# Kernel optimization log

Measured on AMD Instinct MI355X. Metric: run time of the kernel, lower is better.

The kernel has to match this reference:

```python
import jax, jax.numpy as jnp
import numpy as np

N_EMBD = 1024
N_HEAD = 16
B, T = 2, 2048
EPS_LN = 1e-5
EPS_RENORM = 1e-8


def _layernorm(x, w, b):
    mu = jnp.mean(x, axis=-1, keepdims=True)
    var = jnp.mean(jnp.square(x - mu), axis=-1, keepdims=True)
    return (x - mu) * jax.lax.rsqrt(var + EPS_LN) * w + b


def setup_inputs() -> dict:
    key = jax.random.key(0)
    ks = jax.random.split(key, 8)
    C = N_EMBD
    s = 0.02
    return {
        "x": jax.random.normal(ks[0], (B, T, C), jnp.float32),
        "ln1_w": jnp.ones((C,), jnp.float32),
        "ln1_b": jnp.zeros((C,), jnp.float32),
        "w_attn": jax.random.normal(ks[1], (C, 3 * C), jnp.float32) * s,
        "b_attn": jnp.zeros((3 * C,), jnp.float32),
        "w_attn_proj": jax.random.normal(ks[2], (C, C), jnp.float32) * s,
        "b_attn_proj": jnp.zeros((C,), jnp.float32),
        "threshold": jnp.full((N_HEAD,), 0.01, jnp.float32),
        "leak": jnp.full((N_HEAD,), 2.0, jnp.float32),
        "steepness": jnp.full((N_HEAD,), 2.0, jnp.float32),
        "ln2_w": jnp.ones((C,), jnp.float32),
        "ln2_b": jnp.zeros((C,), jnp.float32),
        "w_fc": jax.random.normal(ks[3], (C, 4 * C), jnp.float32) * s,
        "b_fc": jnp.zeros((4 * C,), jnp.float32),
        "w_mlp_proj": jax.random.normal(ks[4], (4 * C, C), jnp.float32) * s,
        "b_mlp_proj": jnp.zeros((C,), jnp.float32),
    }


def _ember_block(x, ln1_w, ln1_b, w_attn, b_attn, w_attn_proj, b_attn_proj,
                 threshold, leak, steepness, ln2_w, ln2_b,
                 w_fc, b_fc, w_mlp_proj, b_mlp_proj):
    Bx, Tx, C = x.shape
    H = N_HEAD
    D = C // H

    h = _layernorm(x, ln1_w, ln1_b)
    qkv = h @ w_attn + b_attn                      # [B,T,3C]
    q, k, v = jnp.split(qkv, 3, axis=-1)
    q = q.reshape(Bx, Tx, H, D).transpose(0, 2, 1, 3)  # [B,H,T,D]
    k = k.reshape(Bx, Tx, H, D).transpose(0, 2, 1, 3)
    v = v.reshape(Bx, Tx, H, D).transpose(0, 2, 1, 3)

    att = jnp.einsum('bhqd,bhkd->bhqk', q, k) * (1.0 / np.sqrt(D))
    causal = jnp.tril(jnp.ones((Tx, Tx), bool))
    att = jnp.where(causal[None, None], att, -jnp.inf)
    p = jax.nn.softmax(att, axis=-1)               # [B,H,T,T]

    # per-head LIF gating
    th = (jnp.abs(threshold) * 0.1)[None, :, None, None]
    lk = jax.nn.sigmoid(leak)[None, :, None, None]
    st = jax.nn.softplus(steepness)[None, :, None, None]
    fire = jax.nn.sigmoid(st * (p - th))
    w = fire + lk * (1.0 - fire)
    m = p * w
    m = m / (jnp.sum(m, axis=-1, keepdims=True) + EPS_RENORM)

    y = jnp.einsum('bhqk,bhkd->bhqd', m, v)
    y = y.transpose(0, 2, 1, 3).reshape(Bx, Tx, C)
    y = y @ w_attn_proj + b_attn_proj
    x = x + y

    h2 = _layernorm(x, ln2_w, ln2_b)
    h2 = jax.nn.gelu(h2 @ w_fc + b_fc, approximate=False)
    x = x + (h2 @ w_mlp_proj + b_mlp_proj)
    return x


def reference(x, ln1_w, ln1_b, w_attn, b_attn, w_attn_proj, b_attn_proj,
              threshold, leak, steepness, ln2_w, ln2_b,
              w_fc, b_fc, w_mlp_proj, b_mlp_proj):
    return _ember_block(x, ln1_w, ln1_b, w_attn, b_attn, w_attn_proj, b_attn_proj,
                        threshold, leak, steepness, ln2_w, ln2_b,
                        w_fc, b_fc, w_mlp_proj, b_mlp_proj)
```

## Files before the change

### kernel.cpp

```cpp
#include <hip/hip_runtime.h>
#include <hip/hip_bf16.h>
#include <math.h>

typedef __bf16 bf16_t;
typedef __bf16 bf16x8 __attribute__((ext_vector_type(8)));
typedef __bf16 bf16x4 __attribute__((ext_vector_type(4)));
typedef float  f32x4  __attribute__((ext_vector_type(4)));
typedef unsigned int u32;

static constexpr int C_    = 1024;
static constexpr int NH    = 16;
static constexpr int DH    = 64;
static constexpr int BB    = 2;
static constexpr int TT    = 2048;
static constexpr int MROWS = BB * TT;
static constexpr float LOG2E = 1.4426950408889634f;

__device__ __forceinline__ void gload_lds16(const bf16_t* src, bf16_t* dst) {
  __builtin_amdgcn_global_load_lds(
      (const __attribute__((address_space(1))) u32*)(src),
      (__attribute__((address_space(3))) u32*)(dst),
      16, 0, 0);
}

__device__ __forceinline__ u32 cvt_pk_bf16(float a, float b) {
  u32 r;
  asm("v_cvt_pk_bf16_f32 %0, %1, %2" : "=v"(r) : "v"(a), "v"(b));
  return r;
}

__device__ __forceinline__ float fexp2(float x) {
#if __has_builtin(__builtin_amdgcn_exp2f)
  return __builtin_amdgcn_exp2f(x);
#else
  return exp2f(x);
#endif
}
__device__ __forceinline__ float frcp(float x) {
#if __has_builtin(__builtin_amdgcn_rcpf)
  return __builtin_amdgcn_rcpf(x);
#else
  return 1.0f / x;
#endif
}

__device__ __forceinline__ int sc_to_t(int s, int c) {
  if (s < 32)  return s;
  if (s < 64)  return 32 + (s - 32) * 2 + c;
  if (s < 96)  return 96 + (s - 64) * 3 + c;
  return 192 + (s - 96) * 4 + c;
}

__device__ __forceinline__ void item40_to_uc(int t, int& u, int& c) {
  if (t < 4)       { u = t;                c = 0; }
  else if (t < 12) { int v = t - 4;  u = 4  + (v >> 1); c = v & 1; }
  else if (t < 24) { int v = t - 12; u = 8  + v / 3;    c = v - 3 * (v / 3); }
  else             { int v = t - 24; u = 12 + (v >> 2); c = v & 3; }
}

__global__ __launch_bounds__(256) void ln_bf16(
    const float* __restrict__ x, const float* __restrict__ w,
    const float* __restrict__ b, bf16_t* __restrict__ out)
{
  const int row = blockIdx.x;
  const int tid = threadIdx.x;
  const float4 v = reinterpret_cast<const float4*>(x + (size_t)row * C_)[tid];
  float s  = v.x + v.y + v.z + v.w;
  float s2 = v.x*v.x + v.y*v.y + v.z*v.z + v.w*v.w;
#pragma unroll
  for (int m = 1; m < 64; m <<= 1) { s += __shfl_xor(s, m); s2 += __shfl_xor(s2, m); }
  __shared__ float red[8];
  const int wv = tid >> 6;
  if ((tid & 63) == 0) { red[wv] = s; red[4 + wv] = s2; }
  __syncthreads();
  s  = red[0] + red[1] + red[2] + red[3];
  s2 = red[4] + red[5] + red[6] + red[7];
  const float mu   = s * (1.0f / C_);
  const float rstd = rsqrtf(s2 * (1.0f / C_) - mu * mu + 1e-5f);
  const float4 wv4 = reinterpret_cast<const float4*>(w)[tid];
  const float4 bv4 = reinterpret_cast<const float4*>(b)[tid];
  bf16x4 o;
  o[0] = (bf16_t)((v.x - mu) * rstd * wv4.x + bv4.x);
  o[1] = (bf16_t)((v.y - mu) * rstd * wv4.y + bv4.y);
  o[2] = (bf16_t)((v.z - mu) * rstd * wv4.z + bv4.z);
  o[3] = (bf16_t)((v.w - mu) * rstd * wv4.w + bv4.w);
  *reinterpret_cast<bf16x4*>(out + (size_t)row * C_ + tid * 4) = o;
}

__global__ __launch_bounds__(256) void ln2_fuse(
    const float* __restrict__ p0, const bf16_t* __restrict__ p1,
    const float* __restrict__ xin, const float* __restrict__ pbias,
    const float* __restrict__ w, const float* __restrict__ b,
    float* __restrict__ x2out, bf16_t* __restrict__ out)
{
  const int row = blockIdx.x;
  const int tid = threadIdx.x;
  const size_t base = (size_t)row * C_ + tid * 4;
  const float4 v0 = *reinterpret_cast<const float4*>(p0 + base);
  const bf16x4 v1 = *reinterpret_cast<const bf16x4*>(p1 + base);
  const float4 xr = *reinterpret_cast<const float4*>(xin + base);
  const float4 pb = *reinterpret_cast<const float4*>(pbias + tid * 4);
  float4 v;
  v.x = v0.x + (float)v1[0] + pb.x + xr.x;
  v.y = v0.y + (float)v1[1] + pb.y + xr.y;
  v.z = v0.z + (float)v1[2] + pb.z + xr.z;
  v.w = v0.w + (float)v1[3] + pb.w + xr.w;
  *reinterpret_cast<float4*>(x2out + base) = v;

  float s  = v.x + v.y + v.z + v.w;
  float s2 = v.x*v.x + v.y*v.y + v.z*v.z + v.w*v.w;
#pragma unroll
  for (int m = 1; m < 64; m <<= 1) { s += __shfl_xor(s, m); s2 += __shfl_xor(s2, m); }
  __shared__ float red[8];
  const int wv = tid >> 6;
  if ((tid & 63) == 0) { red[wv] = s; red[4 + wv] = s2; }
  __syncthreads();
  s  = red[0] + red[1] + red[2] + red[3];
  s2 = red[4] + red[5] + red[6] + red[7];
  const float mu   = s * (1.0f / C_);
  const float rstd = rsqrtf(s2 * (1.0f / C_) - mu * mu + 1e-5f);
  const float4 wv4 = reinterpret_cast<const float4*>(w)[tid];
  const float4 bv4 = reinterpret_cast<const float4*>(b)[tid];
  bf16x4 o;
  o[0] = (bf16_t)((v.x - mu) * rstd * wv4.x + bv4.x);
  o[1] = (bf16_t)((v.y - mu) * rstd * wv4.y + bv4.y);
  o[2] = (bf16_t)((v.z - mu) * rstd * wv4.z + bv4.z);
  o[3] = (bf16_t)((v.w - mu) * rstd * wv4.w + bv4.w);
  *reinterpret_cast<bf16x4*>(out + base) = o;
}

__global__ __launch_bounds__(256) void combine3(
    float* __restrict__ out, const bf16_t* __restrict__ p1,
    const bf16_t* __restrict__ p2, const bf16_t* __restrict__ p3,
    const float* __restrict__ bias, const float* __restrict__ resid)
{
  const size_t idx = ((size_t)blockIdx.x * 256 + threadIdx.x) * 4;
  float4 o = *reinterpret_cast<const float4*>(out + idx);
  const bf16x4 a = *reinterpret_cast<const bf16x4*>(p1 + idx);
  const bf16x4 b = *reinterpret_cast<const bf16x4*>(p2 + idx);
  const bf16x4 c = *reinterpret_cast<const bf16x4*>(p3 + idx);
  const float4 r = *reinterpret_cast<const float4*>(resid + idx);
  const int col = (int)(idx & (C_ - 1));
  const float4 bv = *reinterpret_cast<const float4*>(bias + col);
  o.x += (float)a[0] + (float)b[0] + (float)c[0] + bv.x + r.x;
  o.y += (float)a[1] + (float)b[1] + (float)c[1] + bv.y + r.y;
  o.z += (float)a[2] + (float)b[2] + (float)c[2] + bv.z + r.z;
  o.w += (float)a[3] + (float)b[3] + (float)c[3] + bv.w + r.w;
  *reinterpret_cast<float4*>(out + idx) = o;
}

__global__ __launch_bounds__(256) void transpose_w(
    const float* __restrict__ in, bf16_t* __restrict__ out, int K, int N)
{
  __shared__ float tile[32][33];
  const int tx = threadIdx.x & 31, ty = threadIdx.x >> 5;
  const int n0 = blockIdx.x * 32, k0 = blockIdx.y * 32;
#pragma unroll
  for (int i = 0; i < 4; ++i)
    tile[ty + i * 8][tx] = in[(size_t)(k0 + ty + i * 8) * N + n0 + tx];
  __syncthreads();
#pragma unroll
  for (int i = 0; i < 4; ++i)
    out[(size_t)(n0 + ty + i * 8) * K + k0 + tx] = (bf16_t)tile[tx][ty + i * 8];
}

template<int EPI>
__global__ __launch_bounds__(512, 1) void gemmP(
    const bf16_t* __restrict__ A, const bf16_t* __restrict__ Bt,
    const float* __restrict__ bias, float* __restrict__ fout,
    bf16_t* __restrict__ bout0, bf16_t* __restrict__ bout1,
    bf16_t* __restrict__ bout2, int N, int Kc, int Kfull, int nbn)
{
  __shared__ bf16_t As[3][256 * 64];
  __shared__ bf16_t Bs[3][128 * 64];
  const int tid  = threadIdx.x;
  const int wave = tid >> 6, lane = tid & 63;
  const int r = lane & 15, g = lane >> 4;
  const int wm = wave >> 2, wn = wave & 3;

  const int cpx = gridDim.x >> 3;
  const int swz = (blockIdx.x & 7) * cpx + (blockIdx.x >> 3);
  const int bm = swz / nbn, bn = swz - bm * nbn;
  const int z  = blockIdx.z;
  const int k0 = z * Kc;

  const bf16_t* Abase = A  + (size_t)bm * 256 * Kfull + k0;
  const bf16_t* Bbase = Bt + (size_t)bn * 128 * Kfull + k0;

  f32x4 acc[8][2] = {};

  auto STG_A = [&](int buf, int kt, int pass) {
    const int idx = pass * 512 + tid;
    const int rr = idx >> 3, cc = idx & 7, gs = cc ^ (rr & 7);
    gload_lds16(Abase + (size_t)rr * Kfull + kt + gs * 8, &As[buf][idx * 8]);
  };
  auto STG_B = [&](int buf, int kt, int pass) {
    const int idx = pass * 512 + tid;
    const int rr = idx >> 3, cc = idx & 7, gs = cc ^ (rr & 7);
    gload_lds16(Bbase + (size_t)rr * Kfull + kt + gs * 8, &Bs[buf][idx * 8]);
  };
  auto STAGE6 = [&](int buf, int kt) {
    STG_A(buf, kt, 0); STG_A(buf, kt, 1);
    STG_A(buf, kt, 2); STG_A(buf, kt, 3);
    STG_B(buf, kt, 0); STG_B(buf, kt, 1);
  };

  const int NT = Kc >> 6;
  STAGE6(0, 0);
  STAGE6(1, 64);

  for (int t = 0; t < NT; ++t) {
    const int buf = t % 3;
    if (t + 1 < NT) asm volatile("s_waitcnt vmcnt(6)" ::: "memory");
    else            asm volatile("s_waitcnt vmcnt(0)" ::: "memory");
    __builtin_amdgcn_s_barrier();
    asm volatile("" ::: "memory");

    const bool pre = (t + 2 < NT);
    const int kn   = (t + 2) << 6;
    const int bnx  = (t + 2) % 3;

    bf16x8 bfr[2][2];
#pragma unroll
    for (int s2 = 0; s2 < 2; ++s2)
#pragma unroll
      for (int ni = 0; ni < 2; ++ni) {
        const int rr = wn * 32 + ni * 16 + r;
        bfr[s2][ni] = *reinterpret_cast<const bf16x8*>(
            &Bs[buf][rr * 64 + (((s2 << 2) | g) ^ (rr & 7)) * 8]);
      }
#pragma unroll
    for (int mh = 0; mh < 2; ++mh) {
      bf16x8 af[2][4];
#pragma unroll
      for (int s2 = 0; s2 < 2; ++s2)
#pragma unroll
        for (int mi = 0; mi < 4; ++mi) {
          const int rr = wm * 128 + (mh * 4 + mi) * 16 + r;
          af[s2][mi] = *reinterpret_cast<const bf16x8*>(
              &As[buf][rr * 64 + (((s2 << 2) | g) ^ (rr & 7)) * 8]);
        }
      if (pre) {
        if (mh == 0) { STG_A(bnx, kn, 0); STG_A(bnx, kn, 1); STG_A(bnx, kn, 2); }
        else         { STG_A(bnx, kn, 3); STG_B(bnx, kn, 0); STG_B(bnx, kn, 1); }
      }
      __builtin_amdgcn_s_setprio(1);
#pragma unroll
      for (int s2 = 0; s2 < 2; ++s2)
#pragma unroll
        for (int mi = 0; mi < 4; ++mi)
#pragma unroll
          for (int ni = 0; ni < 2; ++ni)
            acc[mh * 4 + mi][ni] = __builtin_amdgcn_mfma_f32_16x16x32_bf16(
                af[s2][mi], bfr[s2][ni], acc[mh * 4 + mi][ni], 0, 0, 0);
      __builtin_amdgcn_s_setprio(0);
    }
  }

#pragma unroll
  for (int mi = 0; mi < 8; ++mi) {
#pragma unroll
    for (int ni = 0; ni < 2; ++ni) {
      const int grow0 = bm * 256 + wm * 128 + mi * 16 + g * 4;
      const int gcol  = bn * 128 + wn * 32 + ni * 16 + r;
      const float bv = bias[gcol];
#pragma unroll
      for (int i = 0; i < 4; ++i) {
        const int grow = grow0 + i;
        const float v = acc[mi][ni][i] + bv;
        if constexpr (EPI == 0) {
          const int which = gcol >> 10;
          const int c0 = gcol & 1023;
          const int hh = c0 >> 6, dd = c0 & 63;
          const int bb = grow >> 11, tt = grow & 2047;
          if (which == 2)
            bout2[((size_t)(bb * NH + hh) * DH + dd) * TT + tt] = (bf16_t)v;
          else {
            bf16_t* dst = (which == 0) ? bout0 : bout1;
            dst[((size_t)(bb * NH + hh) * TT + tt) * DH + dd] = (bf16_t)v;
          }
        } else {
          const float gl = 0.5f * v * (1.0f + erff(v * 0.70710678118654752f));
          bout0[(size_t)grow * N + gcol] = (bf16_t)gl;
        }
      }
    }
  }
}

__global__ __launch_bounds__(256) void gemm_sk(
    const bf16_t* __restrict__ A, const bf16_t* __restrict__ Bt,
    float* __restrict__ fout, bf16_t* __restrict__ bout0,
    bf16_t* __restrict__ bout1, bf16_t* __restrict__ bout2,
    int M, int N, int Kc, int Kfull)
{
  constexpr int BM = 128, BN = 128, BK = 64;
  __shared__ bf16_t As[BM * BK];
  __shared__ bf16_t Bs[BN * BK];
  const int tid  = threadIdx.x;
  const int wave = tid >> 6, lane = tid & 63;
  const int r = lane & 15, g = lane >> 4;
  const int wm = wave >> 1, wn = wave & 1;
  const int bm = blockIdx.x, bn = blockIdx.y;
  const int z  = blockIdx.z;
  const int kstart = z * Kc;

  const bf16_t* Abase = A  + (size_t)bm * BM * Kfull;
  const bf16_t* Bbase = Bt + (size_t)bn * BN * Kfull;

  f32x4 acc[4][4] = {};

  for (int kt = kstart; kt < kstart + Kc; kt += BK) {
#pragma unroll
    for (int it = 0; it < 4; ++it) {
      const int c0 = it * 256 + wave * 64;
      const int idx = c0 + lane;
      const int rr = idx >> 3, cc = idx & 7;
      const int gs = cc ^ (rr & 7);
      gload_lds16(Abase + (size_t)rr * Kfull + kt + gs * 8, As + c0 * 8);
    }
#pragma unroll
    for (int it = 0; it < 4; ++it) {
      const int c0 = it * 256 + wave * 64;
      const int idx = c0 + lane;
      const int rr = idx >> 3, cc = idx & 7;
      const int gs = cc ^ (rr & 7);
      gload_lds16(Bbase + (size_t)rr * Kfull + kt + gs * 8, Bs + c0 * 8);
    }
    asm volatile("s_waitcnt vmcnt(0)" ::: "memory");
    __syncthreads();
#pragma unroll
    for (int s = 0; s < 2; ++s) {
      bf16x8 af[4], bfr[4];
#pragma unroll
      for (int mi = 0; mi < 4; ++mi) {
        const int rr = wm * 64 + mi * 16 + r;
        const int ch = (s * 4 + g) ^ (rr & 7);
        af[mi] = *reinterpret_cast<const bf16x8*>(&As[rr * BK + ch * 8]);
      }
#pragma unroll
      for (int ni = 0; ni < 4; ++ni) {
        const int rr = wn * 64 + ni * 16 + r;
        const int ch = (s * 4 + g) ^ (rr & 7);
        bfr[ni] = *reinterpret_cast<const bf16x8*>(&Bs[rr * BK + ch * 8]);
      }
#pragma unroll
      for (int mi = 0; mi < 4; ++mi)
#pragma unroll
        for (int ni = 0; ni < 4; ++ni)
          acc[mi][ni] = __builtin_amdgcn_mfma_f32_16x16x32_bf16(
              af[mi], bfr[ni], acc[mi][ni], 0, 0, 0);
    }
    __syncthreads();
  }

#pragma unroll
  for (int mi = 0; mi < 4; ++mi) {
#pragma unroll
    for (int ni = 0; ni < 4; ++ni) {
      const int grow0 = bm * BM + wm * 64 + mi * 16 + g * 4;
      const int gcol  = bn * BN + wn * 64 + ni * 16 + r;
#pragma unroll
      for (int i = 0; i < 4; ++i) {
        const int grow = grow0 + i;
        const float v = acc[mi][ni][i];
        const size_t o = (size_t)grow * N + gcol;
        if (z == 0) fout[o] = v;
        else {
          bf16_t* pb = (z == 1) ? bout0 : (z == 2) ? bout1 : bout2;
          pb[o] = (bf16_t)v;
        }
      }
    }
  }
}


__global__ __launch_bounds__(512, 4) void attn_p1(
    const bf16_t* __restrict__ Q, const bf16_t* __restrict__ Km,
    float2* __restrict__ mzP)
{
  __shared__ bf16_t Ks[2][64 * 64];
  const int tid = threadIdx.x;
  const int w = tid >> 6, lane = tid & 63;
  const int r = lane & 15, g = lane >> 4;
  const int bid = blockIdx.x;
  const int bh  = (bid & 7) * 4 + ((bid >> 3) & 3);
  int gu, c; item40_to_uc(bid >> 5, gu, c);
  const int cmax = gu >> 2;
  const bool diag = (c == cmax);
  const int nt = diag ? ((gu & 3) * 2 + 2) : 8;
  const int s = gu * 8 + w;
  const int qrow = gu * 128 + w * 16 + r;

  const bf16_t* Qh = Q  + (size_t)bh * TT * DH;
  const bf16_t* Kh = Km + (size_t)bh * TT * DH;
  const float SCL = 0.125f * LOG2E;

  bf16x8 qf[2];
#pragma unroll
  for (int s2 = 0; s2 < 2; ++s2) {
    bf16x8 t = *reinterpret_cast<const bf16x8*>(Qh + (size_t)qrow * DH + s2 * 32 + g * 8);
#pragma unroll
    for (int i = 0; i < 8; ++i) t[i] = (bf16_t)((float)t[i] * SCL);
    qf[s2] = t;
  }

  auto STAGEK = [&](int b, int t8) {
    const int rr = tid >> 3, cc = tid & 7, gs = cc ^ (rr & 7);
    gload_lds16(Kh + (size_t)(c * 512 + t8 * 64 + rr) * DH + gs * 8, &Ks[b][tid * 8]);
  };

  float runM = -1e30f, runZ = 0.f;
  STAGEK(0, 0);
  for (int t8 = 0; t8 < nt; ++t8) {
    const int b = t8 & 1;
    asm volatile("s_waitcnt vmcnt(0)" ::: "memory");
    __syncthreads();
    if (t8 + 1 < nt) STAGEK(b ^ 1, t8 + 1);
    f32x4 sfT[4] = {};
#pragma unroll
    for (int s2 = 0; s2 < 2; ++s2) {
      bf16x8 kf[4];
#pragma unroll
      for (int ni = 0; ni < 4; ++ni)
        kf[ni] = *reinterpret_cast<const bf16x8*>(
            &Ks[b][(ni * 16 + r) * 64 + (((s2 << 2) | g) ^ (r & 7)) * 8]);
#pragma unroll
      for (int ni = 0; ni < 4; ++ni)
        sfT[ni] = __builtin_amdgcn_mfma_f32_16x16x32_bf16(kf[ni], qf[s2], sfT[ni], 0, 0, 0);
    }
    const int kbase = c * 512 + t8 * 64;
    float xv[16];
#pragma unroll
    for (int ni = 0; ni < 4; ++ni)
#pragma unroll
      for (int j = 0; j < 4; ++j) {
        float x = sfT[ni][j];
        if (diag) {
          const int kcol = kbase + ni * 16 + g * 4 + j;
          if (kcol > qrow) x = -1e30f;
        }
        xv[ni * 4 + j] = x;
      }
    float nm = runM;
#pragma unroll
    for (int e = 0; e < 16; ++e) nm = fmaxf(nm, xv[e]);
    float z = runZ * fexp2(runM - nm);
#pragma unroll
    for (int e = 0; e < 16; ++e) z += fexp2(xv[e] - nm);
    runM = nm; runZ = z;
  }
#pragma unroll
  for (int msk = 16; msk < 64; msk <<= 1) {
    const float om = __shfl_xor(runM, msk), oz = __shfl_xor(runZ, msk);
    const float nm = fmaxf(runM, om);
    runZ = runZ * fexp2(runM - nm) + oz * fexp2(om - nm);
    runM = nm;
  }
  if (lane < 16)
    mzP[((size_t)(bh * 128 + s) * 4 + c) * 16 + r] = make_float2(runM, runZ);
}

__global__ __launch_bounds__(512, 2) void attn_p3(
    const bf16_t* __restrict__ Q, const bf16_t* __restrict__ Km,
    const bf16_t* __restrict__ Vt, const float2* __restrict__ mzP,
    bf16_t* __restrict__ Y, uint2* __restrict__ yaccA,
    uint2* __restrict__ yaccB, float* __restrict__ denP,
    const float* __restrict__ thrp, const float* __restrict__ leakp,
    const float* __restrict__ steepp)
{
  __shared__ bf16_t Ks[2][64 * 64];
  __shared__ bf16_t Vs[2][64 * 64];
  __shared__ __align__(16) u32 Ms[8][512];

  const int tid = threadIdx.x;
  const int w = tid >> 6, lane = tid & 63;
  const int r = lane & 15, g = lane >> 4;
  const int bid = blockIdx.x;
  const int bh  = (bid & 7) * 4 + ((bid >> 3) & 3);
  int gu, c; item40_to_uc(bid >> 5, gu, c);
  const int cmax = gu >> 2;
  const bool diag = (c == cmax);
  const int nt = diag ? ((gu & 3) * 2 + 2) : 8;
  const int nch = cmax + 1;
  const int s = gu * 8 + w;
  const int row0w = gu * 128 + w * 16;
  const int qrow = row0w + r;
  const int hh = bh & (NH - 1), bb = bh >> 4;

  const bf16_t* Qh  = Q  + (size_t)bh * TT * DH;
  const bf16_t* Kh  = Km + (size_t)bh * TT * DH;
  const bf16_t* Vth = Vt + (size_t)bh * TT * DH;

  const float lk  = 1.0f / (1.0f + expf(-leakp[hh]));
  const float ilk = 1.0f - lk;
  const float st  = log1pf(expf(steepp[hh]));
  const float Lst = LOG2E * st;
  const float A0  = Lst * (fabsf(thrp[hh]) * 0.1f);

  float M = -1e30f, Z = 0.f;
  for (int c2 = 0; c2 < nch; ++c2) {
    const float2 mz = mzP[((size_t)(bh * 128 + s) * 4 + c2) * 16 + r];
    const float nm = fmaxf(M, mz.x);
    Z = Z * fexp2(M - nm) + mz.y * fexp2(mz.x - nm);
    M = nm;
  }
  const float rcpZ = frcp(Z);

  const float SCL = 0.125f * LOG2E;
  bf16x8 qf[2];
#pragma unroll
  for (int s2 = 0; s2 < 2; ++s2) {
    bf16x8 t = *reinterpret_cast<const bf16x8*>(Qh + (size_t)qrow * DH + s2 * 32 + g * 8);
#pragma unroll
    for (int i = 0; i < 8; ++i) t[i] = (bf16_t)((float)t[i] * SCL);
    qf[s2] = t;
  }
  bf16x8 ones;
#pragma unroll
  for (int i = 0; i < 8; ++i) ones[i] = (bf16_t)1.0f;

  uint2* MsU2 = reinterpret_cast<uint2*>(&Ms[w][0]);
  uint4* MsU4 = reinterpret_cast<uint4*>(&Ms[w][0]);

  auto STAGE = [&](int b, int t8) {
    const int kbase = c * 512 + t8 * 64;
    const int rr = tid >> 3, cc = tid & 7, gs = cc ^ (rr & 7);
    gload_lds16(Kh + (size_t)(kbase + rr) * DH + gs * 8, &Ks[b][tid * 8]);
    gload_lds16(Vth + (size_t)rr * TT + kbase + gs * 8, &Vs[b][tid * 8]);
  };

  f32x4 yacc[4] = {};
  f32x4 dacc = {};

  STAGE(0, 0);
  for (int t8 = 0; t8 < nt; ++t8) {
    const int b = t8 & 1;
    asm volatile("s_waitcnt vmcnt(0)" ::: "memory");
    __syncthreads();
    if (t8 + 1 < nt) STAGE(b ^ 1, t8 + 1);
    const int kbase = c * 512 + t8 * 64;
    f32x4 sfT[4] = {};
#pragma unroll
    for (int s2 = 0; s2 < 2; ++s2) {
      bf16x8 kf[4];
#pragma unroll
      for (int ni = 0; ni < 4; ++ni)
        kf[ni] = *reinterpret_cast<const bf16x8*>(
            &Ks[b][(ni * 16 + r) * 64 + (((s2 << 2) | g) ^ (r & 7)) * 8]);
#pragma unroll
      for (int ni = 0; ni < 4; ++ni)
        sfT[ni] = __builtin_amdgcn_mfma_f32_16x16x32_bf16(kf[ni], qf[s2], sfT[ni], 0, 0, 0);
    }
#pragma unroll
    for (int ni = 0; ni < 4; ++ni) {
      float mv[4];
#pragma unroll
      for (int j = 0; j < 4; ++j) {
        float x = sfT[ni][j];
        if (diag) {
          const int kcol = kbase + ni * 16 + g * 4 + j;
          if (kcol > qrow) x = -1e30f;
        }
        const float p    = fexp2(x - M) * rcpZ;
        const float fire = frcp(1.0f + fexp2(A0 - Lst * p));
        mv[j] = p * fmaf(ilk, fire, lk);
      }
      MsU2[r * 16 + ((4 * ni + g) ^ ((r & 7) << 1))] =
          make_uint2(cvt_pk_bf16(mv[0], mv[1]), cvt_pk_bf16(mv[2], mv[3]));
    }
#pragma unroll
    for (int s2 = 0; s2 < 2; ++s2) {
      const uint4 aw = MsU4[r * 8 + ((s2 * 4 + g) ^ (r & 7))];
      const bf16x8 af = __builtin_bit_cast(bf16x8, aw);
      bf16x8 vf[4];
#pragma unroll
      for (int ni = 0; ni < 4; ++ni)
        vf[ni] = *reinterpret_cast<const bf16x8*>(
            &Vs[b][(ni * 16 + r) * 64 + (((s2 << 2) | g) ^ (r & 7)) * 8]);
#pragma unroll
      for (int ni = 0; ni < 4; ++ni)
        yacc[ni] = __builtin_amdgcn_mfma_f32_16x16x32_bf16(af, vf[ni], yacc[ni], 0, 0, 0);
      dacc = __builtin_amdgcn_mfma_f32_16x16x32_bf16(af, ones, dacc, 0, 0, 0);
    }
  }

  if (nch == 1) {
#pragma unroll
    for (int j = 0; j < 4; ++j) {
      const float rd = frcp(dacc[j] + 1e-8f);
      const int t = row0w + g * 4 + j;
#pragma unroll
      for (int ni = 0; ni < 4; ++ni)
        Y[((size_t)(bb * TT + t)) * C_ + hh * DH + ni * 16 + r] =
            (bf16_t)(yacc[ni][j] * rd);
    }
  } else {
    const int pid = bh * 288 + (sc_to_t(s, c) - 32);
    uint2* pb = (pid < 4096) ? (yaccA + (size_t)pid * 256)
                             : (yaccB + (size_t)(pid - 4096) * 256);
#pragma unroll
    for (int ni = 0; ni < 4; ++ni)
      pb[ni * 64 + lane] =
          make_uint2(cvt_pk_bf16(yacc[ni][0], yacc[ni][1]),
                     cvt_pk_bf16(yacc[ni][2], yacc[ni][3]));
    if (r == 0)
      *reinterpret_cast<float4*>(&denP[(size_t)pid * 16 + g * 4]) =
          make_float4(dacc[0], dacc[1], dacc[2], dacc[3]);
  }
}

__global__ __launch_bounds__(256) void attn_p4(
    const uint2* __restrict__ yaccA, const uint2* __restrict__ yaccB,
    const float* __restrict__ denP, bf16_t* __restrict__ Y)
{
  const int bid = blockIdx.x;
  const int bh  = bid / 96;
  const int s   = 32 + (bid - bh * 96);
  const int nch = (s >> 5) + 1;
  const int hh = bh & (NH - 1), bb = bh >> 4;

  const int tid = threadIdx.x;
  const int w = tid >> 6, lane = tid & 63;
  const int r = lane & 15, g = lane >> 4;

  float acc[4] = {};
  float den[4] = {};
  for (int c = 0; c < nch; ++c) {
    const int pid = bh * 288 + (sc_to_t(s, c) - 32);
    const uint2* pb = (pid < 4096) ? (yaccA + (size_t)pid * 256)
                                   : (yaccB + (size_t)(pid - 4096) * 256);
    const uint2 u = pb[w * 64 + lane];
    acc[0] += __builtin_bit_cast(float, (u.x & 0xFFFFu) << 16);
    acc[1] += __builtin_bit_cast(float, (u.x & 0xFFFF0000u));
    acc[2] += __builtin_bit_cast(float, (u.y & 0xFFFFu) << 16);
    acc[3] += __builtin_bit_cast(float, (u.y & 0xFFFF0000u));
    const float4 d4 = *reinterpret_cast<const float4*>(&denP[(size_t)pid * 16 + g * 4]);
    den[0] += d4.x; den[1] += d4.y; den[2] += d4.z; den[3] += d4.w;
  }
#pragma unroll
  for (int j = 0; j < 4; ++j) {
    const float rd = 1.0f / (den[j] + 1e-8f);
    const int t = s * 16 + g * 4 + j;
    Y[((size_t)(bb * TT + t)) * C_ + hh * DH + w * 16 + r] = (bf16_t)(acc[j] * rd);
  }
}

extern "C" void kernel_launch(void* const* d_in, const int* in_sizes, int n_in,
                              void* d_out, int out_size, void* d_ws, size_t ws_size,
                              hipStream_t stream)
{
  const float* x      = (const float*)d_in[0];
  const float* ln1_w  = (const float*)d_in[1];
  const float* ln1_b  = (const float*)d_in[2];
  const float* w_attn = (const float*)d_in[3];
  const float* b_attn = (const float*)d_in[4];
  const float* w_proj = (const float*)d_in[5];
  const float* b_proj = (const float*)d_in[6];
  const float* thr    = (const float*)d_in[7];
  const float* leak   = (const float*)d_in[8];
  const float* steep  = (const float*)d_in[9];
  const float* ln2_w  = (const float*)d_in[10];
  const float* ln2_b  = (const float*)d_in[11];
  const float* w_fc   = (const float*)d_in[12];
  const float* b_fc   = (const float*)d_in[13];
  const float* w_mlp  = (const float*)d_in[14];
  const float* b_mlp  = (const float*)d_in[15];

  char* ws = (char*)d_ws;
  bf16_t* q    = (bf16_t*)(ws + 0);
  bf16_t* k    = (bf16_t*)(ws + 8388608);
  bf16_t* vT   = (bf16_t*)(ws + 25165824);
  bf16_t* gbuf = (bf16_t*)(ws + 0);
  bf16_t* hbuf = (bf16_t*)(ws + 33554432);
  float*  x2   = (float*) (ws + 41943040);
  bf16_t* wT_attn = (bf16_t*)(ws + 58720256);
  bf16_t* wT_proj = (bf16_t*)(ws + 65011712);
  bf16_t* wT_fc   = (bf16_t*)(ws + 67108864);
  bf16_t* wT_mlp  = (bf16_t*)(ws + 75497472);

  uint2* yaccA = (uint2*)(ws + 16777216);
  uint2* yaccB = (uint2*)(ws + 41943040);
  float* denP  = (float*)(ws + 52428800);
  float2* mzP  = (float2*)(ws + 53477376);

  bf16_t* pp1 = (bf16_t*)(ws + 0);
  bf16_t* mp1 = (bf16_t*)(ws + 33554432);
  bf16_t* mp2 = (bf16_t*)(ws + 58720256);
  bf16_t* mp3 = (bf16_t*)(ws + 67108864);

  float* out = (float*)d_out;

  ln_bf16<<<dim3(MROWS), dim3(256), 0, stream>>>(x, ln1_w, ln1_b, hbuf);
  transpose_w<<<dim3(96, 32),  dim3(256), 0, stream>>>(w_attn, wT_attn, 1024, 3072);
  transpose_w<<<dim3(32, 32),  dim3(256), 0, stream>>>(w_proj, wT_proj, 1024, 1024);
  transpose_w<<<dim3(128, 32), dim3(256), 0, stream>>>(w_fc,   wT_fc,   1024, 4096);
  transpose_w<<<dim3(32, 128), dim3(256), 0, stream>>>(w_mlp,  wT_mlp,  4096, 1024);

  gemmP<0><<<dim3(384, 1, 1), dim3(512), 0, stream>>>(
      hbuf, wT_attn, b_attn, nullptr, q, k, vT, 3072, 1024, 1024, 24);

  attn_p1<<<dim3(1280), dim3(512), 0, stream>>>(q, k, mzP);
  attn_p3<<<dim3(1280), dim3(512), 0, stream>>>(
      q, k, vT, mzP, hbuf, yaccA, yaccB, denP, thr, leak, steep);
  attn_p4<<<dim3(3072), dim3(256), 0, stream>>>(yaccA, yaccB, denP, hbuf);

  gemm_sk<<<dim3(32, 8, 2), dim3(256), 0, stream>>>(
      hbuf, wT_proj, x2, pp1, nullptr, nullptr, MROWS, 1024, 512, 1024);

  ln2_fuse<<<dim3(MROWS), dim3(256), 0, stream>>>(
      x2, pp1, x, b_proj, ln2_w, ln2_b, x2, hbuf);

  gemmP<2><<<dim3(512, 1, 1), dim3(512), 0, stream>>>(
      hbuf, wT_fc, b_fc, nullptr, gbuf, nullptr, nullptr, 4096, 1024, 1024, 32);

  gemm_sk<<<dim3(32, 8, 4), dim3(256), 0, stream>>>(
      gbuf, wT_mlp, out, mp1, mp2, mp3, MROWS, 1024, 1024, 4096);

  combine3<<<dim3(4096), dim3(256), 0, stream>>>(out, mp1, mp2, mp3, b_mlp, x2);
}
```

Measured before the change: 309.4 us.

## Shrink attention blocks to 64 rows, fuse prep kernels, add separate V transpose

Merges the LN1 and four weight-transpose launches into one prep kernel. The attention kernels go from 512-thread blocks covering 128 query rows to 256-thread blocks covering 64 rows, doubling the grid and raising occupancy. Causal masking is now applied only on the last diagonal tile. The QKV GEMM now writes V in the same row layout as Q and K and a new kernel transposes it, replacing strided scattered stores with an extra pass. This risks more K/V reloads per block and an additional launch, and the attn_p4/partial-buffer indexing must still match the new item mapping.

```diff
diff --git a/kernel.cpp b/kernel.cpp
--- a/kernel.cpp
+++ b/kernel.cpp
@@ -51,40 +51,64 @@
   return 192 + (s - 96) * 4 + c;
 }
 
-__device__ __forceinline__ void item40_to_uc(int t, int& u, int& c) {
-  if (t < 4)       { u = t;                c = 0; }
-  else if (t < 12) { int v = t - 4;  u = 4  + (v >> 1); c = v & 1; }
-  else if (t < 24) { int v = t - 12; u = 8  + v / 3;    c = v - 3 * (v / 3); }
-  else             { int v = t - 24; u = 12 + (v >> 2); c = v & 3; }
-}
-
-__global__ __launch_bounds__(256) void ln_bf16(
-    const float* __restrict__ x, const float* __restrict__ w,
-    const float* __restrict__ b, bf16_t* __restrict__ out)
-{
-  const int row = blockIdx.x;
+__device__ __forceinline__ void item64_to_uc(int item, int& u, int& c) {
+  if (item < 8)       { u = item;               c = 0; }
+  else if (item < 24) { int v = item - 8;  u = 8  + (v >> 1); c = v & 1; }
+  else if (item < 48) { int v = item - 24; u = 16 + v / 3;    c = v - 3 * (v / 3); }
+  else                { int v = item - 48; u = 24 + (v >> 2); c = v & 3; }
+}
+
+__global__ __launch_bounds__(256) void prep(
+    const float* __restrict__ x, const float* __restrict__ ln1_w,
+    const float* __restrict__ ln1_b, bf16_t* __restrict__ hout,
+    const float* __restrict__ w_attn, bf16_t* __restrict__ wT_attn,
+    const float* __restrict__ w_proj, bf16_t* __restrict__ wT_proj,
+    const float* __restrict__ w_fc,   bf16_t* __restrict__ wT_fc,
+    const float* __restrict__ w_mlp,  bf16_t* __restrict__ wT_mlp)
+{
+  const int bid = blockIdx.x;
   const int tid = threadIdx.x;
-  const float4 v = reinterpret_cast<const float4*>(x + (size_t)row * C_)[tid];
-  float s  = v.x + v.y + v.z + v.w;
-  float s2 = v.x*v.x + v.y*v.y + v.z*v.z + v.w*v.w;
-#pragma unroll
-  for (int m = 1; m < 64; m <<= 1) { s += __shfl_xor(s, m); s2 += __shfl_xor(s2, m); }
-  __shared__ float red[8];
-  const int wv = tid >> 6;
-  if ((tid & 63) == 0) { red[wv] = s; red[4 + wv] = s2; }
+  if (bid < MROWS) {
+    const int row = bid;
+    const float4 v = reinterpret_cast<const float4*>(x + (size_t)row * C_)[tid];
+    float s  = v.x + v.y + v.z + v.w;
+    float s2 = v.x*v.x + v.y*v.y + v.z*v.z + v.w*v.w;
+#pragma unroll
+    for (int m = 1; m < 64; m <<= 1) { s += __shfl_xor(s, m); s2 += __shfl_xor(s2, m); }
+    __shared__ float red[8];
+    const int wv = tid >> 6;
+    if ((tid & 63) == 0) { red[wv] = s; red[4 + wv] = s2; }
+    __syncthreads();
+    s  = red[0] + red[1] + red[2] + red[3];
+    s2 = red[4] + red[5] + red[6] + red[7];
+    const float mu   = s * (1.0f / C_);
+    const float rstd = rsqrtf(s2 * (1.0f / C_) - mu * mu + 1e-5f);
+    const float4 wv4 = reinterpret_cast<const float4*>(ln1_w)[tid];
+    const float4 bv4 = reinterpret_cast<const float4*>(ln1_b)[tid];
+    bf16x4 o;
+    o[0] = (bf16_t)((v.x - mu) * rstd * wv4.x + bv4.x);
+    o[1] = (bf16_t)((v.y - mu) * rstd * wv4.y + bv4.y);
+    o[2] = (bf16_t)((v.z - mu) * rstd * wv4.z + bv4.z);
+    o[3] = (bf16_t)((v.w - mu) * rstd * wv4.w + bv4.w);
+    *reinterpret_cast<bf16x4*>(hout + (size_t)row * C_ + tid * 4) = o;
+    return;
+  }
+  int tb = bid - MROWS;
+  const float* in; bf16_t* out; int K, N, nbx;
+  if (tb < 3072)      { in = w_attn; out = wT_attn; K = 1024; N = 3072; nbx = 96; }
+  else if (tb < 4096) { tb -= 3072; in = w_proj; out = wT_proj; K = 1024; N = 1024; nbx = 32; }
+  else if (tb < 8192) { tb -= 4096; in = w_fc;   out = wT_fc;   K = 1024; N = 4096; nbx = 128; }
+  else                { tb -= 8192; in = w_mlp;  out = wT_mlp;  K = 4096; N = 1024; nbx = 32; }
+  const int n0 = (tb % nbx) * 32, k0 = (tb / nbx) * 32;
+  __shared__ float tile[32][33];
+  const int tx = tid & 31, ty = tid >> 5;
+#pragma unroll
+  for (int i = 0; i < 4; ++i)
+    tile[ty + i * 8][tx] = in[(size_t)(k0 + ty + i * 8) * N + n0 + tx];
   __syncthreads();
-  s  = red[0] + red[1] + red[2] + red[3];
-  s2 = red[4] + red[5] + red[6] + red[7];
-  const float mu   = s * (1.0f / C_);
-  const float rstd = rsqrtf(s2 * (1.0f / C_) - mu * mu + 1e-5f);
-  const float4 wv4 = reinterpret_cast<const float4*>(w)[tid];
-  const float4 bv4 = reinterpret_cast<const float4*>(b)[tid];
-  bf16x4 o;
-  o[0] = (bf16_t)((v.x - mu) * rstd * wv4.x + bv4.x);
-  o[1] = (bf16_t)((v.y - mu) * rstd * wv4.y + bv4.y);
-  o[2] = (bf16_t)((v.z - mu) * rstd * wv4.z + bv4.z);
-  o[3] = (bf16_t)((v.w - mu) * rstd * wv4.w + bv4.w);
-  *reinterpret_cast<bf16x4*>(out + (size_t)row * C_ + tid * 4) = o;
+#pragma unroll
+  for (int i = 0; i < 4; ++i)
+    out[(size_t)(n0 + ty + i * 8) * K + k0 + tx] = (bf16_t)tile[tx][ty + i * 8];
 }
 
 __global__ __launch_bounds__(256) void ln2_fuse(
@@ -149,19 +173,22 @@
   *reinterpret_cast<float4*>(out + idx) = o;
 }
 
-__global__ __launch_bounds__(256) void transpose_w(
-    const float* __restrict__ in, bf16_t* __restrict__ out, int K, int N)
-{
-  __shared__ float tile[32][33];
+__global__ __launch_bounds__(256) void transpose_v(
+    const bf16_t* __restrict__ in, bf16_t* __restrict__ out)
+{
+  __shared__ bf16_t tile[32][33];
+  const int bh = blockIdx.z;
+  const bf16_t* src = in  + (size_t)bh * TT * DH;
+  bf16_t*       dst = out + (size_t)bh * TT * DH;
   const int tx = threadIdx.x & 31, ty = threadIdx.x >> 5;
-  const int n0 = blockIdx.x * 32, k0 = blockIdx.y * 32;
+  const int t0 = blockIdx.x * 32, d0 = blockIdx.y * 32;
 #pragma unroll
   for (int i = 0; i < 4; ++i)
-    tile[ty + i * 8][tx] = in[(size_t)(k0 + ty + i * 8) * N + n0 + tx];
+    tile[ty + i * 8][tx] = src[(size_t)(t0 + ty + i * 8) * DH + d0 + tx];
   __syncthreads();
 #pragma unroll
   for (int i = 0; i < 4; ++i)
-    out[(size_t)(n0 + ty + i * 8) * K + k0 + tx] = (bf16_t)tile[tx][ty + i * 8];
+    dst[(size_t)(d0 + ty + i * 8) * TT + t0 + tx] = tile[tx][ty + i * 8];
 }
 
 template<int EPI>
@@ -181,8 +208,7 @@
   const int cpx = gridDim.x >> 3;
   const int swz = (blockIdx.x & 7) * cpx + (blockIdx.x >> 3);
   const int bm = swz / nbn, bn = swz - bm * nbn;
-  const int z  = blockIdx.z;
-  const int k0 = z * Kc;
+  const int k0 = 0;
 
   const bf16_t* Abase = A  + (size_t)bm * 256 * Kfull + k0;
   const bf16_t* Bbase = Bt + (size_t)bn * 128 * Kfull + k0;
@@ -273,12 +299,8 @@
           const int c0 = gcol & 1023;
           const int hh = c0 >> 6, dd = c0 & 63;
           const int bb = grow >> 11, tt = grow & 2047;
-          if (which == 2)
-            bout2[((size_t)(bb * NH + hh) * DH + dd) * TT + tt] = (bf16_t)v;
-          else {
-            bf16_t* dst = (which == 0) ? bout0 : bout1;
-            dst[((size_t)(bb * NH + hh) * TT + tt) * DH + dd] = (bf16_t)v;
-          }
+          bf16_t* dst = (which == 0) ? bout0 : (which == 1) ? bout1 : bout2;
+          dst[((size_t)(bb * NH + hh) * TT + tt) * DH + dd] = (bf16_t)v;
         } else {
           const float gl = 0.5f * v * (1.0f + erff(v * 0.70710678118654752f));
           bout0[(size_t)grow * N + gcol] = (bf16_t)gl;
@@ -376,7 +398,7 @@
 }
 
 
-__global__ __launch_bounds__(512, 4) void attn_p1(
+__global__ __launch_bounds__(256, 4) void attn_p1(
     const bf16_t* __restrict__ Q, const bf16_t* __restrict__ Km,
     float2* __restrict__ mzP)
 {
@@ -386,12 +408,13 @@
   const int r = lane & 15, g = lane >> 4;
   const int bid = blockIdx.x;
   const int bh  = (bid & 7) * 4 + ((bid >> 3) & 3);
-  int gu, c; item40_to_uc(bid >> 5, gu, c);
-  const int cmax = gu >> 2;
+  int u, c; item64_to_uc(bid >> 5, u, c);
+  const int cmax = u >> 3;
   const bool diag = (c == cmax);
-  const int nt = diag ? ((gu & 3) * 2 + 2) : 8;
-  const int s = gu * 8 + w;
-  const int qrow = gu * 128 + w * 16 + r;
+  const int nt = diag ? (u & 7) + 1 : 8;
+  const int s = 4 * u + w;
+  const int row0 = u * 64 + w * 16;
+  const int qrow = row0 + r;
 
   const bf16_t* Qh = Q  + (size_t)bh * TT * DH;
   const bf16_t* Kh = Km + (size_t)bh * TT * DH;
@@ -407,8 +430,12 @@
   }
 
   auto STAGEK = [&](int b, int t8) {
-    const int rr = tid >> 3, cc = tid & 7, gs = cc ^ (rr & 7);
-    gload_lds16(Kh + (size_t)(c * 512 + t8 * 64 + rr) * DH + gs * 8, &Ks[b][tid * 8]);
+#pragma unroll
+    for (int it = 0; it < 2; ++it) {
+      const int idx = it * 256 + tid;
+      const int rr = idx >> 3, cc = idx & 7, gs = cc ^ (rr & 7);
+      gload_lds16(Kh + (size_t)(c * 512 + t8 * 64 + rr) * DH + gs * 8, &Ks[b][idx * 8]);
+    }
   };
 
   float runM = -1e30f, runZ = 0.f;
@@ -430,6 +457,7 @@
       for (int ni = 0; ni < 4; ++ni)
         sfT[ni] = __builtin_amdgcn_mfma_f32_16x16x32_bf16(kf[ni], qf[s2], sfT[ni], 0, 0, 0);
     }
+    const bool dm = diag && (t8 == nt - 1);
     const int kbase = c * 512 + t8 * 64;
     float xv[16];
 #pragma unroll
@@ -437,7 +465,7 @@
 #pragma unroll
       for (int j = 0; j < 4; ++j) {
         float x = sfT[ni][j];
-        if (diag) {
+        if (dm) {
           const int kcol = kbase + ni * 16 + g * 4 + j;
           if (kcol > qrow) x = -1e30f;
         }
@@ -462,7 +490,7 @@
     mzP[((size_t)(bh * 128 + s) * 4 + c) * 16 + r] = make_float2(runM, runZ);
 }
 
-__global__ __launch_bounds__(512, 2) void attn_p3(
+__global__ __launch_bounds__(256, 4) void attn_p3(
     const bf16_t* __restrict__ Q, const bf16_t* __restrict__ Km,
     const bf16_t* __restrict__ Vt, const float2* __restrict__ mzP,
     bf16_t* __restrict__ Y, uint2* __restrict__ yaccA,
@@ -472,21 +500,21 @@
 {
   __shared__ bf16_t Ks[2][64 * 64];
   __shared__ bf16_t Vs[2][64 * 64];
-  __shared__ __align__(16) u32 Ms[8][512];
+  __shared__ __align__(16) u32 Ms[4][512];
 
   const int tid = threadIdx.x;
   const int w = tid >> 6, lane = tid & 63;
   const int r = lane & 15, g = lane >> 4;
   const int bid = blockIdx.x;
   const int bh  = (bid & 7) * 4 + ((bid >> 3) & 3);
-  int gu, c; item40_to_uc(bid >> 5, gu, c);
-  const int cmax = gu >> 2;
+  int u, c; item64_to_uc(bid >> 5, u, c);
+  const int cmax = u >> 3;
   const bool diag = (c == cmax);
-  const int nt = diag ? ((gu & 3) * 2 + 2) : 8;
+  const int nt = diag ? (u & 7) + 1 : 8;
   const int nch = cmax + 1;
-  const int s = gu * 8 + w;
-  const int row0w = gu * 128 + w * 16;
-  const int qrow = row0w + r;
+  const int s = 4 * u + w;
+  const int row0 = u * 64 + w * 16;
+  const int qrow = row0 + r;
   const int hh = bh & (NH - 1), bb = bh >> 4;
 
   const bf16_t* Qh  = Q  + (size_t)bh * TT * DH;
@@ -526,9 +554,13 @@
 
   auto STAGE = [&](int b, int t8) {
     const int kbase = c * 512 + t8 * 64;
-    const int rr = tid >> 3, cc = tid & 7, gs = cc ^ (rr & 7);
-    gload_lds16(Kh + (size_t)(kbase + rr) * DH + gs * 8, &Ks[b][tid * 8]);
-    gload_lds16(Vth + (size_t)rr * TT + kbase + gs * 8, &Vs[b][tid * 8]);
+#pragma unroll
+    for (int it = 0; it < 2; ++it) {
+      const int idx = it * 256 + tid;
+      const int rr = idx >> 3, cc = idx & 7, gs = cc ^ (rr & 7);
+      gload_lds16(Kh + (size_t)(kbase + rr) * DH + gs * 8, &Ks[b][idx * 8]);
+      gload_lds16(Vth + (size_t)rr * TT + kbase + gs * 8, &Vs[b][idx * 8]);
+    }
   };
 
   f32x4 yacc[4] = {};
@@ -553,13 +585,14 @@
       for (int ni = 0; ni < 4; ++ni)
         sfT[ni] = __builtin_amdgcn_mfma_f32_16x16x32_bf16(kf[ni], qf[s2], sfT[ni], 0, 0, 0);
     }
+    const bool dm = diag && (t8 == nt - 1);
 #pragma unroll
     for (int ni = 0; ni < 4; ++ni) {
       float mv[4];
 #pragma unroll
       for (int j = 0; j < 4; ++j) {
         float x = sfT[ni][j];
-        if (diag) {
+        if (dm) {
           const int kcol = kbase + ni * 16 + g * 4 + j;
           if (kcol > qrow) x = -1e30f;
         }
@@ -590,7 +623,7 @@
 #pragma unroll
     for (int j = 0; j < 4; ++j) {
       const float rd = frcp(dacc[j] + 1e-8f);
-      const int t = row0w + g * 4 + j;
+      const int t = row0 + g * 4 + j;
 #pragma unroll
       for (int ni = 0; ni < 4; ++ni)
         Y[((size_t)(bb * TT + t)) * C_ + hh * DH + ni * 16 + r] =
@@ -671,6 +704,7 @@
   char* ws = (char*)d_ws;
   bf16_t* q    = (bf16_t*)(ws + 0);
   bf16_t* k    = (bf16_t*)(ws + 8388608);
+  bf16_t* v    = (bf16_t*)(ws + 16777216);
   bf16_t* vT   = (bf16_t*)(ws + 25165824);
   bf16_t* gbuf = (bf16_t*)(ws + 0);
   bf16_t* hbuf = (bf16_t*)(ws + 33554432);
@@ -692,17 +726,16 @@
 
   float* out = (float*)d_out;
 
-  ln_bf16<<<dim3(MROWS), dim3(256), 0, stream>>>(x, ln1_w, ln1_b, hbuf);
-  transpose_w<<<dim3(96, 32),  dim3(256), 0, stream>>>(w_attn, wT_attn, 1024, 3072);
-  transpose_w<<<dim3(32, 32),  dim3(256), 0, stream>>>(w_proj, wT_proj, 1024, 1024);
-  transpose_w<<<dim3(128, 32), dim3(256), 0, stream>>>(w_fc,   wT_fc,   1024, 4096);
-  transpose_w<<<dim3(32, 128), dim3(256), 0, stream>>>(w_mlp,  wT_mlp,  4096, 1024);
+  prep<<<dim3(MROWS + 12288), dim3(256), 0, stream>>>(
+      x, ln1_w, ln1_b, hbuf,
+      w_attn, wT_attn, w_proj, wT_proj, w_fc, wT_fc, w_mlp, wT_mlp);
 
   gemmP<0><<<dim3(384, 1, 1), dim3(512), 0, stream>>>(
-      hbuf, wT_attn, b_attn, nullptr, q, k, vT, 3072, 1024, 1024, 24);
-
-  attn_p1<<<dim3(1280), dim3(512), 0, stream>>>(q, k, mzP);
-  attn_p3<<<dim3(1280), dim3(512), 0, stream>>>(
+      hbuf, wT_attn, b_attn, nullptr, q, k, v, 3072, 1024, 1024, 24);
+  transpose_v<<<dim3(64, 2, 32), dim3(256), 0, stream>>>(v, vT);
+
+  attn_p1<<<dim3(2560), dim3(256), 0, stream>>>(q, k, mzP);
+  attn_p3<<<dim3(2560), dim3(256), 0, stream>>>(
       q, k, vT, mzP, hbuf, yaccA, yaccB, denP, thr, leak, steep);
   attn_p4<<<dim3(3072), dim3(256), 0, stream>>>(yaccA, yaccB, denP, hbuf);
 
```

Result: faster. 288.2 us (-6.9%).
